# Kernel optimization log

Measured on AMD Instinct MI355X. Metric: run time of the kernel, lower is better.

The kernel has to match this reference:

```python
import jax, jax.numpy as jnp
import numpy as np

GRID = 64
DX = 1.0 / GRID            # grid spacing (buffer dx)
RADIUS = 2.5 * DX          # search_radius = dx * 2.5
CIN, COUT = 16, 16
B, N = 2, 8192
EPS = 1e-12
FOUR_OVER_PI = 4.0 / np.pi


def _safe_sqrt(v):
    return jnp.sqrt(jnp.maximum(v, EPS))


def _sphere_to_cylinder(x, y, z):
    # volume-preserving map: unit ball -> cylinder (radius 1, height 2)
    sq = x * x + y * y + z * z
    norm = _safe_sqrt(sq)
    xy2 = x * x + y * y
    cap = 1.25 * z * z > xy2                      # polar-cap region
    s_cap = jnp.sqrt(3.0 * norm / (norm + jnp.abs(z) + EPS))
    s_side = norm / _safe_sqrt(xy2)
    xc = jnp.where(cap, x * s_cap, x * s_side)
    yc = jnp.where(cap, y * s_cap, y * s_side)
    zc = jnp.where(cap, jnp.sign(z) * norm, 1.5 * z)
    zero = sq <= EPS
    z0 = jnp.zeros_like(x)
    return (jnp.where(zero, z0, xc), jnp.where(zero, z0, yc), jnp.where(zero, z0, zc))


def _cylinder_to_cube(x, y, z):
    # area-preserving disc -> square on the xy cross-section
    xy2 = x * x + y * y
    nxy = _safe_sqrt(xy2)
    xdom = jnp.abs(y) <= jnp.abs(x)
    safe_x = jnp.where(jnp.abs(x) > EPS, x, 1.0)
    safe_y = jnp.where(jnp.abs(y) > EPS, y, 1.0)
    tx = jnp.sign(x) * nxy
    ty = jnp.sign(y) * nxy
    xa, ya = tx, tx * FOUR_OVER_PI * jnp.arctan(y / safe_x)
    xb, yb = ty * FOUR_OVER_PI * jnp.arctan(x / safe_y), ty
    xc = jnp.where(xdom, xa, xb)
    yc = jnp.where(xdom, ya, yb)
    zero = xy2 <= EPS
    z0 = jnp.zeros_like(x)
    return jnp.where(zero, z0, xc), jnp.where(zero, z0, yc), z


def _cconv_forward(input, pos, weights, grid_pos):
    Bb, C, D, H, Wd = input.shape
    Np = pos.shape[1]
    # [B,C,D,H,W] -> [B,D,H,W,C] -> [B,G,C]  (matches permute+view in torch)
    feat = jnp.transpose(input, (0, 2, 3, 4, 1)).reshape(Bb, D * H * Wd, C)
    # fixed 6^3 stencil of candidate grid cells around each point
    off = jnp.arange(6) - 2
    o0, o1, o2 = jnp.meshgrid(off, off, off, indexing='ij')
    offs = jnp.stack([o0, o1, o2], axis=-1).reshape(-1, 3)          # [216,3]
    base = jnp.floor(pos / DX).astype(jnp.int32)                    # [B,N,3]
    cand = base[:, :, None, :] + offs[None, None]                   # [B,N,216,3]
    dims = jnp.array([D, H, Wd])
    in_bounds = jnp.all((cand >= 0) & (cand < dims), axis=-1)       # [B,N,216]
    cc = jnp.clip(cand, 0, dims - 1)
    flat = (cc[..., 0] * H + cc[..., 1]) * Wd + cc[..., 2]          # [B,N,216]
    bidx = jnp.arange(Bb)[:, None, None]
    npos = grid_pos[flat]                                           # [B,N,216,3]
    fg = feat[bidx, flat]                                           # [B,N,216,C]
    rel = npos - pos[:, :, None, :]
    dist2 = jnp.sum(rel * rel, axis=-1)
    valid = in_bounds & (dist2 <= RADIUS * RADIUS)
    # map relative offsets (scaled to the unit ball) to the unit cube
    u = rel / RADIUS
    x, y, z = _sphere_to_cylinder(u[..., 0], u[..., 1], u[..., 2])
    x, y, z = _cylinder_to_cube(x, y, z)
    # linear interpolation of the 3x3x3 kernel, align_corners=True -> coords in [0,2]
    taps = jnp.arange(3, dtype=pos.dtype)
    def hat(c):
        c = jnp.clip((c * 0.5 + 0.5) * 2.0, 0.0, 2.0)
        return jnp.maximum(0.0, 1.0 - jnp.abs(c[..., None] - taps))  # [B,N,216,3]
    w0, w1, w2 = hat(x), hat(y), hat(z)
    w27 = jnp.einsum('bnki,bnkj,bnkl->bnkijl', w0, w1, w2).reshape(Bb, Np, -1, 27)
    w27 = w27 * valid[..., None].astype(w27.dtype)
    # accumulate interpolated features per kernel tap, then apply the kernel
    acc = jnp.einsum('bnkt,bnkc->bntc', w27, fg)                    # [B,N,27,C]
    out = jnp.einsum('bntc,tcd->bnd', acc, weights.reshape(27, C, -1))
    # normalize=True (Open3D default): divide by neighbor count
    count = jnp.sum(valid, axis=-1).astype(out.dtype)
    out = out / jnp.maximum(count, 1.0)[..., None]
    return out


def setup_inputs() -> dict:
    key = jax.random.key(0)
    k1, k2, k3 = jax.random.split(key, 3)
    inp = jax.random.normal(k1, (B, CIN, GRID, GRID, GRID), jnp.float32)
    pos = jax.random.uniform(k2, (B, N, 3), jnp.float32)
    weights = jax.random.normal(k3, (3, 3, 3, CIN, COUT), jnp.float32) * 0.05
    ax = jnp.arange(GRID, dtype=jnp.float32) * DX
    g = jnp.stack(jnp.meshgrid(ax, ax, ax, indexing='ij'), axis=-1).reshape(-1, 3)
    return {"input": inp, "pos": pos, "weights": weights, "grid_pos": g}


def reference(input, pos, weights, grid_pos):
    return _cconv_forward(input, pos, weights, grid_pos)
```

## Files before the change

### kernel.cpp

```cpp
#include <hip/hip_runtime.h>
#include <cstdint>

namespace {
constexpr int kG = 262144;
constexpr int kB = 2;
constexpr int kN = 8192;
constexpr int kPts = kB * kN;
constexpr float kDX = 1.0f / 64.0f;
constexpr float kRad2 = 0.00152587890625f;
constexpr float kInvRad = 25.6f;
constexpr float kEps = 1e-12f;
constexpr float kFourOverPi = 1.27323954473516268615f;

constexpr int PPB = 4;
constexpr int THREADS = PPB * 64;
constexpr int MAXREC = 88;
constexpr int SLOT = 16;
constexpr int GSTRIDE = MAXREC * SLOT + 4;
}

__device__ __forceinline__ float sgnf(float v) {
    return (v > 0.f) ? 1.f : ((v < 0.f) ? -1.f : 0.f);
}

__global__ __launch_bounds__(256) void transpose_feat_k(const float* __restrict__ in,
                                                        float* __restrict__ feat) {
    int idx = blockIdx.x * 256 + threadIdx.x;
    if (idx >= kB * kG) return;
    int b = idx >> 18;
    int g = idx & (kG - 1);
    float v[16];
#pragma unroll
    for (int c = 0; c < 16; ++c) v[c] = in[((size_t)(b * 16 + c)) * kG + g];
    float4* dst = reinterpret_cast<float4*>(feat + (size_t)idx * 16);
    dst[0] = make_float4(v[0], v[1], v[2], v[3]);
    dst[1] = make_float4(v[4], v[5], v[6], v[7]);
    dst[2] = make_float4(v[8], v[9], v[10], v[11]);
    dst[3] = make_float4(v[12], v[13], v[14], v[15]);
}

__global__ __launch_bounds__(THREADS) void cconv_main(
    const float* __restrict__ input, const float* __restrict__ pos,
    const float* __restrict__ W, const float* __restrict__ feat,
    float* __restrict__ out, int use_feat)
{
    __shared__ __align__(16) float rec[PPB * GSTRIDE];

    const int tid = threadIdx.x;
    const int wv = tid >> 6;
    const int lane = tid & 63;
    const int sg = lane >> 4;
    const int lig = lane & 15;
    const int pt = blockIdx.x * PPB + wv;
    const int b = pt >> 13;

    const float px = pos[pt * 3 + 0];
    const float py = pos[pt * 3 + 1];
    const float pz = pos[pt * 3 + 2];
    const int bx = (int)floorf(px * 64.f);
    const int by = (int)floorf(py * 64.f);
    const int bz = (int)floorf(pz * 64.f);

    float* grec = rec + wv * GSTRIDE;
    int nv = 0;

#pragma unroll
    for (int it = 0; it < 4; ++it) {
        int k = it * 64 + lane;
        bool valid = false;
        float rx = 0.f, ry = 0.f, rz = 0.f;
        int flat = 0;
        if (k < 216) {
            int a = k / 36;
            int r = k - a * 36;
            int b1 = r / 6;
            int c1 = r - b1 * 6;
            int g0 = bx + a - 2, g1 = by + b1 - 2, g2 = bz + c1 - 2;
            bool inb = (g0 >= 0) & (g0 < 64) & (g1 >= 0) & (g1 < 64) &
                       (g2 >= 0) & (g2 < 64);
            int q0 = min(max(g0, 0), 63);
            int q1 = min(max(g1, 0), 63);
            int q2 = min(max(g2, 0), 63);
            flat = (q0 * 64 + q1) * 64 + q2;
            rx = __fsub_rn((float)q0 * kDX, px);
            ry = __fsub_rn((float)q1 * kDX, py);
            rz = __fsub_rn((float)q2 * kDX, pz);
            float d2 = __fadd_rn(__fadd_rn(__fmul_rn(rx, rx), __fmul_rn(ry, ry)),
                                 __fmul_rn(rz, rz));
            valid = inb && (d2 <= kRad2);
        }
        unsigned long long ball = __ballot(valid);
        if (valid) {
            int slot = nv + __popcll(ball & ((1ull << lane) - 1ull));
            *reinterpret_cast<float4*>(grec + slot * SLOT) =
                make_float4(rx, ry, rz, __int_as_float(flat));
        }
        nv += (int)__popcll(ball);
    }
    __builtin_amdgcn_wave_barrier();

    if (lane < 8 && nv + lane < MAXREC) {
        float4 z = make_float4(0.f, 0.f, 0.f, 0.f);
        float4* zp = reinterpret_cast<float4*>(grec + (nv + lane) * SLOT);
        zp[0] = z; zp[1] = z; zp[2] = z; zp[3] = z;
    }

    for (int s = lane; s < nv; s += 64) {
        float* rp = grec + s * SLOT;
        float4 rc = *reinterpret_cast<const float4*>(rp);
        float flat_bits = rc.w;
        float ux = rc.x * kInvRad, uy = rc.y * kInvRad, uz = rc.z * kInvRad;

        float xx = ux * ux, yy = uy * uy, zz = uz * uz;
        float xy2 = xx + yy;
        float sq = xy2 + zz;
        float nrm = __builtin_amdgcn_sqrtf(fmaxf(sq, kEps));
        bool cap = (1.25f * zz > xy2);
        float scap = __builtin_amdgcn_sqrtf(3.f * nrm) *
                     __builtin_amdgcn_rsqf(nrm + fabsf(uz) + kEps);
        float sside = nrm * __builtin_amdgcn_rsqf(fmaxf(xy2, kEps));
        float sc = cap ? scap : sside;
        float xc = ux * sc, yc = uy * sc;
        float zc = cap ? sgnf(uz) * nrm : 1.5f * uz;
        bool z1 = (sq <= kEps);
        if (z1) { xc = 0.f; yc = 0.f; zc = 0.f; }

        float xy2b = xc * xc + yc * yc;
        float nxy = __builtin_amdgcn_sqrtf(fmaxf(xy2b, kEps));
        bool xdom = (fabsf(yc) <= fabsf(xc));
        float num = xdom ? yc : xc;
        float den = xdom ? xc : yc;
        float dsafe = (fabsf(den) > kEps) ? den : 1.0f;
        float r = num * __builtin_amdgcn_rcpf(dsafe);
        float r2 = r * r;
        float at = -0.01172120f;
        at = at * r2 + 0.05265332f;
        at = at * r2 - 0.11643287f;
        at = at * r2 + 0.19354346f;
        at = at * r2 - 0.33262347f;
        at = at * r2 + 0.99997726f;
        at = at * r;
        float tt = sgnf(den) * nxy;
        float g = tt * kFourOverPi * at;
        float xo = xdom ? tt : g;
        float yo = xdom ? g : tt;
        if (xy2b <= kEps) { xo = 0.f; yo = 0.f; }
        float zo = zc;

        float tx = fminf(fmaxf(xo + 1.f, 0.f), 2.f) - 1.f;
        float ty = fminf(fmaxf(yo + 1.f, 0.f), 2.f) - 1.f;
        float tz = fminf(fmaxf(zo + 1.f, 0.f), 2.f) - 1.f;
        float wx0 = fmaxf(0.f, -tx), wx1 = 1.f - fabsf(tx), wx2 = fmaxf(0.f, tx);
        float wy0 = fmaxf(0.f, -ty), wy1 = 1.f - fabsf(ty), wy2 = fmaxf(0.f, ty);
        float wz0 = fmaxf(0.f, -tz), wz1 = 1.f - fabsf(tz), wz2 = fmaxf(0.f, tz);

        float4* rp4 = reinterpret_cast<float4*>(rp);
        rp4[0] = make_float4(wx0 * wy0, wx0 * wy1, wx0 * wy2, wz0);
        rp4[1] = make_float4(wx1 * wy0, wx1 * wy1, wx1 * wy2, wz1);
        rp4[2] = make_float4(wx2 * wy0, wx2 * wy1, wx2 * wy2, wz2);
        rp[12] = flat_bits;
    }
    __builtin_amdgcn_wave_barrier();

    float acc[28];
#pragma unroll
    for (int t = 0; t < 28; ++t) acc[t] = 0.f;

    const float* fbp = use_feat ? (feat + (size_t)b * kG * 16)
                                : (input + (size_t)b * 16 * kG);
    const int nvp = (nv + 3) & ~3;

    const float* rp = grec + sg * SLOT;
    float4 F0 = reinterpret_cast<const float4*>(rp)[0];
    float4 F1 = reinterpret_cast<const float4*>(rp)[1];
    float4 F2 = reinterpret_cast<const float4*>(rp)[2];
    int flat = __float_as_int(rp[12]);
    float f = use_feat ? fbp[(size_t)flat * 16 + lig] : fbp[(size_t)lig * kG + flat];

    for (int s = sg; s < nvp; s += 4) {
        const float* rpn = rp + 4 * SLOT;
        float4 G0 = reinterpret_cast<const float4*>(rpn)[0];
        float4 G1 = reinterpret_cast<const float4*>(rpn)[1];
        float4 G2 = reinterpret_cast<const float4*>(rpn)[2];
        int flatn = __float_as_int(rpn[12]);
        float fn = use_feat ? fbp[(size_t)flatn * 16 + lig]
                            : fbp[(size_t)lig * kG + flatn];
        float m0 = F0.w * f, m1 = F1.w * f, m2 = F2.w * f;
        acc[0]  += F0.x * m0; acc[1]  += F0.x * m1; acc[2]  += F0.x * m2;
        acc[3]  += F0.y * m0; acc[4]  += F0.y * m1; acc[5]  += F0.y * m2;
        acc[6]  += F0.z * m0; acc[7]  += F0.z * m1; acc[8]  += F0.z * m2;
        acc[9]  += F1.x * m0; acc[10] += F1.x * m1; acc[11] += F1.x * m2;
        acc[12] += F1.y * m0; acc[13] += F1.y * m1; acc[14] += F1.y * m2;
        acc[15] += F1.z * m0; acc[16] += F1.z * m1; acc[17] += F1.z * m2;
        acc[18] += F2.x * m0; acc[19] += F2.x * m1; acc[20] += F2.x * m2;
        acc[21] += F2.y * m0; acc[22] += F2.y * m1; acc[23] += F2.y * m2;
        acc[24] += F2.z * m0; acc[25] += F2.z * m1; acc[26] += F2.z * m2;
        F0 = G0; F1 = G1; F2 = G2; f = fn; rp = rpn;
    }

    const bool hi32 = (lane >= 32);
    float kp[14];
#pragma unroll
    for (int j = 0; j < 14; ++j) {
        float send = hi32 ? acc[j] : acc[14 + j];
        float recv = __shfl_xor(send, 32);
        kp[j] = (hi32 ? acc[14 + j] : acc[j]) + recv;
    }
    const bool hi16 = (lane & 16) != 0;
    float kk[7];
#pragma unroll
    for (int j = 0; j < 7; ++j) {
        float send = hi16 ? kp[j] : kp[7 + j];
        float recv = __shfl_xor(send, 16);
        kk[j] = (hi16 ? kp[7 + j] : kp[j]) + recv;
    }

    float partial[16];
#pragma unroll
    for (int d = 0; d < 16; ++d) partial[d] = 0.f;
    const float* wbase = W + (sg * 7) * 256 + lig * 16;
#pragma unroll
    for (int j = 0; j < 7; ++j) {
        if (sg * 7 + j < 27) {
            const float4* wr = reinterpret_cast<const float4*>(wbase + j * 256);
            float4 a0 = wr[0], a1 = wr[1], a2 = wr[2], a3 = wr[3];
            float at_ = kk[j];
            partial[0]  += at_ * a0.x; partial[1]  += at_ * a0.y;
            partial[2]  += at_ * a0.z; partial[3]  += at_ * a0.w;
            partial[4]  += at_ * a1.x; partial[5]  += at_ * a1.y;
            partial[6]  += at_ * a1.z; partial[7]  += at_ * a1.w;
            partial[8]  += at_ * a2.x; partial[9]  += at_ * a2.y;
            partial[10] += at_ * a2.z; partial[11] += at_ * a2.w;
            partial[12] += at_ * a3.x; partial[13] += at_ * a3.y;
            partial[14] += at_ * a3.z; partial[15] += at_ * a3.w;
        }
    }

#pragma unroll
    for (int half = 8; half >= 1; half >>= 1) {
        bool up = (lig & half) != 0;
#pragma unroll
        for (int j = 0; j < half; ++j) {
            float send = up ? partial[j] : partial[j + half];
            float recv = __shfl_xor(send, half);
            partial[j] = (up ? partial[j + half] : partial[j]) + recv;
        }
    }
    float res = partial[0];
    res += __shfl_xor(res, 16);
    res += __shfl_xor(res, 32);
    res = res / fmaxf((float)nv, 1.f);
    if (lane < 16) out[(size_t)pt * 16 + lig] = res;
}

extern "C" void kernel_launch(void* const* d_in, const int* in_sizes, int n_in,
                              void* d_out, int out_size, void* d_ws, size_t ws_size,
                              hipStream_t stream) {
    const float* input = (const float*)d_in[0];
    const float* pos   = (const float*)d_in[1];
    const float* W     = (const float*)d_in[2];
    float* out  = (float*)d_out;
    float* feat = (float*)d_ws;

    const size_t feat_bytes = (size_t)kB * kG * 16 * sizeof(float);
    int use_feat = (d_ws != nullptr && ws_size >= feat_bytes) ? 1 : 0;

    if (use_feat) {
        transpose_feat_k<<<(kB * kG + 255) / 256, 256, 0, stream>>>(input, feat);
    }
    cconv_main<<<kPts / PPB, THREADS, 0, stream>>>(input, pos, W, feat, out, use_feat);
}
```

Before: 84.04 us.

## Prefetch neighbor features four records ahead and compact weight records

Moves the flat grid indices into a separate pre-scaled int array in LDS and issues the feature gathers four neighbor records ahead, hoisted ahead of the weight-computation phase, so global load latency overlaps both that compute and the accumulation loop. Weight records shrink from 16 to 12 floats by storing the nine xy products plus two z weights and recomputing the third z weight in the loop. This adds registers for the four in-flight features and one extra subtract per iteration. It also changes the padding and zeroing logic for the tail records.

```diff
diff --git a/kernel.cpp b/kernel.cpp
--- a/kernel.cpp
+++ b/kernel.cpp
@@ -15,8 +15,9 @@
 constexpr int PPB = 4;
 constexpr int THREADS = PPB * 64;
 constexpr int MAXREC = 88;
-constexpr int SLOT = 16;
-constexpr int GSTRIDE = MAXREC * SLOT + 4;
+constexpr int SLOT = 12;
+constexpr int NFLAT = 108;
+constexpr int GSTRIDE = MAXREC * SLOT + NFLAT + 4;
 }
 
 __device__ __forceinline__ float sgnf(float v) {
@@ -62,6 +63,7 @@
     const int bz = (int)floorf(pz * 64.f);
 
     float* grec = rec + wv * GSTRIDE;
+    int* iflats = reinterpret_cast<int*>(grec + MAXREC * SLOT);
     int nv = 0;
 
 #pragma unroll
@@ -69,7 +71,7 @@
         int k = it * 64 + lane;
         bool valid = false;
         float rx = 0.f, ry = 0.f, rz = 0.f;
-        int flat = 0;
+        int flat16 = 0;
         if (k < 216) {
             int a = k / 36;
             int r = k - a * 36;
@@ -81,7 +83,7 @@
             int q0 = min(max(g0, 0), 63);
             int q1 = min(max(g1, 0), 63);
             int q2 = min(max(g2, 0), 63);
-            flat = (q0 * 64 + q1) * 64 + q2;
+            flat16 = ((q0 * 64 + q1) * 64 + q2) << 4;
             rx = __fsub_rn((float)q0 * kDX, px);
             ry = __fsub_rn((float)q1 * kDX, py);
             rz = __fsub_rn((float)q2 * kDX, pz);
@@ -93,7 +95,8 @@
         if (valid) {
             int slot = nv + __popcll(ball & ((1ull << lane) - 1ull));
             *reinterpret_cast<float4*>(grec + slot * SLOT) =
-                make_float4(rx, ry, rz, __int_as_float(flat));
+                make_float4(rx, ry, rz, 0.f);
+            iflats[slot] = flat16;
         }
         nv += (int)__popcll(ball);
     }
@@ -102,13 +105,25 @@
     if (lane < 8 && nv + lane < MAXREC) {
         float4 z = make_float4(0.f, 0.f, 0.f, 0.f);
         float4* zp = reinterpret_cast<float4*>(grec + (nv + lane) * SLOT);
-        zp[0] = z; zp[1] = z; zp[2] = z; zp[3] = z;
-    }
+        zp[0] = z; zp[1] = z; zp[2] = z;
+    }
+    if (lane < 24 && nv + lane < NFLAT) iflats[nv + lane] = 0;
+    __builtin_amdgcn_wave_barrier();
+
+    const float* fbp = use_feat ? (feat + (size_t)b * kG * 16)
+                                : (input + (size_t)b * 16 * kG);
+    int fl0 = iflats[sg];
+    int fl1 = iflats[sg + 4];
+    int fl2 = iflats[sg + 8];
+    int fl3 = iflats[sg + 12];
+    float f0 = use_feat ? fbp[(size_t)fl0 + lig] : fbp[(size_t)lig * kG + (fl0 >> 4)];
+    float f1 = use_feat ? fbp[(size_t)fl1 + lig] : fbp[(size_t)lig * kG + (fl1 >> 4)];
+    float f2 = use_feat ? fbp[(size_t)fl2 + lig] : fbp[(size_t)lig * kG + (fl2 >> 4)];
+    float f3 = use_feat ? fbp[(size_t)fl3 + lig] : fbp[(size_t)lig * kG + (fl3 >> 4)];
 
     for (int s = lane; s < nv; s += 64) {
         float* rp = grec + s * SLOT;
         float4 rc = *reinterpret_cast<const float4*>(rp);
-        float flat_bits = rc.w;
         float ux = rc.x * kInvRad, uy = rc.y * kInvRad, uz = rc.z * kInvRad;
 
         float xx = ux * ux, yy = uy * uy, zz = uz * uz;
@@ -122,8 +137,7 @@
         float sc = cap ? scap : sside;
         float xc = ux * sc, yc = uy * sc;
         float zc = cap ? sgnf(uz) * nrm : 1.5f * uz;
-        bool z1 = (sq <= kEps);
-        if (z1) { xc = 0.f; yc = 0.f; zc = 0.f; }
+        if (sq <= kEps) { xc = 0.f; yc = 0.f; zc = 0.f; }
 
         float xy2b = xc * xc + yc * yc;
         float nxy = __builtin_amdgcn_sqrtf(fmaxf(xy2b, kEps));
@@ -152,13 +166,12 @@
         float tz = fminf(fmaxf(zo + 1.f, 0.f), 2.f) - 1.f;
         float wx0 = fmaxf(0.f, -tx), wx1 = 1.f - fabsf(tx), wx2 = fmaxf(0.f, tx);
         float wy0 = fmaxf(0.f, -ty), wy1 = 1.f - fabsf(ty), wy2 = fmaxf(0.f, ty);
-        float wz0 = fmaxf(0.f, -tz), wz1 = 1.f - fabsf(tz), wz2 = fmaxf(0.f, tz);
+        float wz0 = fmaxf(0.f, -tz), wz1 = 1.f - fabsf(tz);
 
         float4* rp4 = reinterpret_cast<float4*>(rp);
-        rp4[0] = make_float4(wx0 * wy0, wx0 * wy1, wx0 * wy2, wz0);
-        rp4[1] = make_float4(wx1 * wy0, wx1 * wy1, wx1 * wy2, wz1);
-        rp4[2] = make_float4(wx2 * wy0, wx2 * wy1, wx2 * wy2, wz2);
-        rp[12] = flat_bits;
+        rp4[0] = make_float4(wx0 * wy0, wx0 * wy1, wx0 * wy2, wx1 * wy0);
+        rp4[1] = make_float4(wx1 * wy1, wx1 * wy2, wx2 * wy0, wx2 * wy1);
+        rp4[2] = make_float4(wx2 * wy2, wz0, wz1, 0.f);
     }
     __builtin_amdgcn_wave_barrier();
 
@@ -166,36 +179,35 @@
 #pragma unroll
     for (int t = 0; t < 28; ++t) acc[t] = 0.f;
 
-    const float* fbp = use_feat ? (feat + (size_t)b * kG * 16)
-                                : (input + (size_t)b * 16 * kG);
     const int nvp = (nv + 3) & ~3;
-
     const float* rp = grec + sg * SLOT;
     float4 F0 = reinterpret_cast<const float4*>(rp)[0];
     float4 F1 = reinterpret_cast<const float4*>(rp)[1];
     float4 F2 = reinterpret_cast<const float4*>(rp)[2];
-    int flat = __float_as_int(rp[12]);
-    float f = use_feat ? fbp[(size_t)flat * 16 + lig] : fbp[(size_t)lig * kG + flat];
 
     for (int s = sg; s < nvp; s += 4) {
         const float* rpn = rp + 4 * SLOT;
         float4 G0 = reinterpret_cast<const float4*>(rpn)[0];
         float4 G1 = reinterpret_cast<const float4*>(rpn)[1];
         float4 G2 = reinterpret_cast<const float4*>(rpn)[2];
-        int flatn = __float_as_int(rpn[12]);
-        float fn = use_feat ? fbp[(size_t)flatn * 16 + lig]
-                            : fbp[(size_t)lig * kG + flatn];
-        float m0 = F0.w * f, m1 = F1.w * f, m2 = F2.w * f;
+        int fln = iflats[s + 16];
+        float fnew = use_feat ? fbp[(size_t)fln + lig]
+                              : fbp[(size_t)lig * kG + (fln >> 4)];
+
+        float wz2 = (1.f - F2.y) - F2.z;
+        float m0 = F2.y * f0, m1 = F2.z * f0, m2 = wz2 * f0;
         acc[0]  += F0.x * m0; acc[1]  += F0.x * m1; acc[2]  += F0.x * m2;
         acc[3]  += F0.y * m0; acc[4]  += F0.y * m1; acc[5]  += F0.y * m2;
         acc[6]  += F0.z * m0; acc[7]  += F0.z * m1; acc[8]  += F0.z * m2;
-        acc[9]  += F1.x * m0; acc[10] += F1.x * m1; acc[11] += F1.x * m2;
-        acc[12] += F1.y * m0; acc[13] += F1.y * m1; acc[14] += F1.y * m2;
-        acc[15] += F1.z * m0; acc[16] += F1.z * m1; acc[17] += F1.z * m2;
-        acc[18] += F2.x * m0; acc[19] += F2.x * m1; acc[20] += F2.x * m2;
-        acc[21] += F2.y * m0; acc[22] += F2.y * m1; acc[23] += F2.y * m2;
-        acc[24] += F2.z * m0; acc[25] += F2.z * m1; acc[26] += F2.z * m2;
-        F0 = G0; F1 = G1; F2 = G2; f = fn; rp = rpn;
+        acc[9]  += F0.w * m0; acc[10] += F0.w * m1; acc[11] += F0.w * m2;
+        acc[12] += F1.x * m0; acc[13] += F1.x * m1; acc[14] += F1.x * m2;
+        acc[15] += F1.y * m0; acc[16] += F1.y * m1; acc[17] += F1.y * m2;
+        acc[18] += F1.z * m0; acc[19] += F1.z * m1; acc[20] += F1.z * m2;
+        acc[21] += F1.w * m0; acc[22] += F1.w * m1; acc[23] += F1.w * m2;
+        acc[24] += F2.x * m0; acc[25] += F2.x * m1; acc[26] += F2.x * m2;
+
+        f0 = f1; f1 = f2; f2 = f3; f3 = fnew;
+        F0 = G0; F1 = G1; F2 = G2; rp = rpn;
     }
 
     const bool hi32 = (lane >= 32);
```

Result: faster. 79.62 us (-5.3%).
